# Optimization experiments

Measured on AMD Instinct MI355X. Metric: run time of the kernel, lower is better.

## Reference

```python
import jax, jax.numpy as jnp
import numpy as np

EMB_DIM = 256
Q_DIM = 512
V_DIM = 512

def setup_inputs() -> dict:
    key = jax.random.key(0)
    ks = jax.random.split(key, 7)
    B, S = 8, 2048
    x = jax.random.normal(ks[0], (B, S, EMB_DIM), dtype=jnp.float32)
    s = 1.0 / np.sqrt(EMB_DIM)
    Wq = jax.random.normal(ks[1], (EMB_DIM, Q_DIM), dtype=jnp.float32) * s
    bq = jax.random.normal(ks[2], (Q_DIM,), dtype=jnp.float32) * 0.01
    Wk = jax.random.normal(ks[3], (EMB_DIM, Q_DIM), dtype=jnp.float32) * s
    bk = jax.random.normal(ks[4], (Q_DIM,), dtype=jnp.float32) * 0.01
    Wv = jax.random.normal(ks[5], (EMB_DIM, V_DIM), dtype=jnp.float32) * s
    bv = jax.random.normal(ks[6], (V_DIM,), dtype=jnp.float32) * 0.01
    return {"x": x, "Wq": Wq, "bq": bq, "Wk": Wk, "bk": bk, "Wv": Wv, "bv": bv}

def reference(x, Wq, bq, Wk, bk, Wv, bv):
    # q/k/v projections (torch Linear == x @ W + b with W stored [in, out] here)
    q = jax.nn.sigmoid(jnp.einsum('bse,eq->bsq', x, Wq) + bq)   # [B,S,Q]
    k = jnp.einsum('bse,eq->bsq', x, Wk) + bk                   # [B,S,Q]
    v = jnp.einsum('bse,ev->bsv', x, Wv) + bv                   # [B,S,V]
    scale = 1.0 / jnp.sqrt(jnp.float32(EMB_DIM))
    qk = jnp.einsum('bsq,btq->bst', q, k) * scale               # [B,S,S]
    qk = jax.nn.elu(qk)
    attn = jax.nn.softmax(qk, axis=-1)
    return jnp.einsum('bst,btv->bsv', attn, v)                  # [B,S,V]
```

## Files before the change

### kernel.cpp

```cpp
#include <hip/hip_runtime.h>
#include <hip/hip_bf16.h>
#include <math.h>

typedef unsigned short u16;
using short8 = __attribute__((ext_vector_type(8))) short;
using f32x4  = __attribute__((ext_vector_type(4))) float;

#define BK 32


__device__ __forceinline__ u16 f2bf(float f) {
  union { float f; unsigned u; } v; v.f = f;
  unsigned r = v.u + 0x7FFFu + ((v.u >> 16) & 1u);
  return (u16)(r >> 16);
}

__device__ __forceinline__ float fexp(float x) { return __expf(x); }

__device__ __forceinline__ void gld16(const void* g, void* l) {
  __builtin_amdgcn_global_load_lds(
      (const __attribute__((address_space(1))) void*)g,
      (__attribute__((address_space(3))) void*)l,
      16, 0, 0);
}


__device__ __forceinline__ void gemm_core64(const u16* __restrict__ Ag,
                                            const u16* __restrict__ Bg,
                                            int K, int lda, int ldb,
                                            u16* As, u16* Bs,
                                            f32x4 acc[4][4], int w, int l) {
  const int wm = (w & 1) << 6, wn = (w >> 1) << 6;
  const int ln = l & 15, lq = l >> 4;
  const int sr0 = w * 16 + (l >> 2);
  const int sr1 = 64 + sr0;
  const int skp = (l & 3) * 8;
  const int skg = ((l & 3) ^ ((l >> 3) & 3)) * 8;
  const int kro = (lq ^ ((ln >> 1) & 3)) * 8;

#pragma unroll
  for (int mt = 0; mt < 4; mt++)
#pragma unroll
    for (int nt = 0; nt < 4; nt++) acc[mt][nt] = (f32x4)0.0f;

  for (int k0 = 0; k0 < K; k0 += 64) {
    __syncthreads();
    gld16(Ag + (size_t)sr0 * lda + k0 + skg, As + sr0 * BK + skp);
    gld16(Ag + (size_t)sr1 * lda + k0 + skg, As + sr1 * BK + skp);
    gld16(Ag + (size_t)sr0 * lda + k0 + 32 + skg, As + 4096 + sr0 * BK + skp);
    gld16(Ag + (size_t)sr1 * lda + k0 + 32 + skg, As + 4096 + sr1 * BK + skp);
    gld16(Bg + (size_t)sr0 * ldb + k0 + skg, Bs + sr0 * BK + skp);
    gld16(Bg + (size_t)sr1 * ldb + k0 + skg, Bs + sr1 * BK + skp);
    gld16(Bg + (size_t)sr0 * ldb + k0 + 32 + skg, Bs + 4096 + sr0 * BK + skp);
    gld16(Bg + (size_t)sr1 * ldb + k0 + 32 + skg, Bs + 4096 + sr1 * BK + skp);
    __syncthreads();
#pragma unroll
    for (int h = 0; h < 2; h++) {
      const u16* Ah = As + h * 4096;
      const u16* Bh = Bs + h * 4096;
      short8 af[4], bf[4];
#pragma unroll
      for (int mt = 0; mt < 4; mt++)
        af[mt] = *(const short8*)(Ah + (wm + mt * 16 + ln) * BK + kro);
#pragma unroll
      for (int nt = 0; nt < 4; nt++)
        bf[nt] = *(const short8*)(Bh + (wn + nt * 16 + ln) * BK + kro);
#pragma unroll
      for (int mt = 0; mt < 4; mt++)
#pragma unroll
        for (int nt = 0; nt < 4; nt++)
          acc[mt][nt] = __builtin_amdgcn_mfma_f32_16x16x32_bf16(
              af[mt], bf[nt], acc[mt][nt], 0, 0, 0);
    }
  }
}


__global__ __launch_bounds__(256) void k_conv(
    const float* __restrict__ x, u16* __restrict__ xb,
    const float* __restrict__ Wq, const float* __restrict__ Wk,
    const float* __restrict__ Wv, const float* __restrict__ bq,
    const float* __restrict__ bk, const float* __restrict__ bv,
    u16* __restrict__ Wt, float* __restrict__ bcat,
    float* __restrict__ lsum) {
  const int bid = blockIdx.x;
  if (bid < 4096) {
    int i = bid * 256 + threadIdx.x;
    float4 v = ((const float4*)x)[i];
    ushort4 o;
    o.x = f2bf(v.x); o.y = f2bf(v.y); o.z = f2bf(v.z); o.w = f2bf(v.w);
    ((ushort4*)xb)[i] = o;
  } else if (bid < 5632) {
    int i = (bid - 4096) * 256 + threadIdx.x;
    int nn = i >> 8, e = i & 255;
    int sel = nn >> 9, c = nn & 511;
    const float* W = (sel == 0) ? Wq : (sel == 1) ? Wk : Wv;
    Wt[i] = f2bf(W[e * 512 + c]);
    if (e == 0) {
      const float* bb = (sel == 0) ? bq : (sel == 1) ? bk : bv;
      bcat[nn] = bb[c];
    }
  } else {
    int i = (bid - 5632) * 256 + threadIdx.x;
    lsum[i] = 0.0f;
  }
}


__global__ __launch_bounds__(256) void k_proj(
    const u16* __restrict__ xb, const u16* __restrict__ Wt,
    const float* __restrict__ bcat, u16* __restrict__ qb,
    u16* __restrict__ kb, u16* __restrict__ vtb) {
  __shared__ __align__(16) u16 As8[8 * 4096];
  __shared__ __align__(16) u16 Bs[2 * 4096];
  const int bm = blockIdx.y * 128;
  const int bnq = blockIdx.x;
  const int tid = threadIdx.x, w = tid >> 6, l = tid & 63;
  const int wm = (w & 1) << 6, wn = (w >> 1) << 6;
  const int ln = l & 15, lq = l >> 4;
  const int sr0 = w * 16 + (l >> 2);
  const int sr1 = 64 + sr0;
  const int skp = (l & 3) * 8;
  const int skg = ((l & 3) ^ ((l >> 3) & 3)) * 8;
  const int kro = (lq ^ ((ln >> 1) & 3)) * 8;

#pragma unroll
  for (int kw = 0; kw < 8; kw++) {
    gld16(xb + (size_t)(bm + sr0) * 256 + kw * 32 + skg,
          As8 + kw * 4096 + sr0 * BK + skp);
    gld16(xb + (size_t)(bm + sr1) * 256 + kw * 32 + skg,
          As8 + kw * 4096 + sr1 * BK + skp);
  }

  const int b = bm >> 11, t0 = bm & 2047;
  const int cb = bnq * 128;

  for (int p = 0; p < 3; p++) {
    const u16* Bg = Wt + (size_t)(p * 512 + cb) * 256;
    f32x4 acc[4][4];
#pragma unroll
    for (int mt = 0; mt < 4; mt++)
#pragma unroll
      for (int nt = 0; nt < 4; nt++) acc[mt][nt] = (f32x4)0.0f;

#pragma unroll
    for (int it2 = 0; it2 < 4; it2++) {
      __syncthreads();
      gld16(Bg + (size_t)sr0 * 256 + it2 * 64 + skg, Bs + sr0 * BK + skp);
      gld16(Bg + (size_t)sr1 * 256 + it2 * 64 + skg, Bs + sr1 * BK + skp);
      gld16(Bg + (size_t)sr0 * 256 + it2 * 64 + 32 + skg,
            Bs + 4096 + sr0 * BK + skp);
      gld16(Bg + (size_t)sr1 * 256 + it2 * 64 + 32 + skg,
            Bs + 4096 + sr1 * BK + skp);
      __syncthreads();
#pragma unroll
      for (int h = 0; h < 2; h++) {
        const u16* Aw = As8 + (it2 * 2 + h) * 4096;
        const u16* Bh = Bs + h * 4096;
        short8 af[4], bf[4];
#pragma unroll
        for (int mt = 0; mt < 4; mt++)
          af[mt] = *(const short8*)(Aw + (wm + mt * 16 + ln) * BK + kro);
#pragma unroll
        for (int nt = 0; nt < 4; nt++)
          bf[nt] = *(const short8*)(Bh + (wn + nt * 16 + ln) * BK + kro);
#pragma unroll
        for (int mt = 0; mt < 4; mt++)
#pragma unroll
          for (int nt = 0; nt < 4; nt++)
            acc[mt][nt] = __builtin_amdgcn_mfma_f32_16x16x32_bf16(
                af[mt], bf[nt], acc[mt][nt], 0, 0, 0);
      }
    }

    if (p < 2) {
      u16* dst = p ? kb : qb;
#pragma unroll
      for (int mt = 0; mt < 4; mt++)
#pragma unroll
        for (int r = 0; r < 4; r++) {
          int row = bm + wm + mt * 16 + lq * 4 + r;
          ushort4 o;
#pragma unroll
          for (int nt = 0; nt < 4; nt++) {
            int col = wn + nt * 16 + ln;
            float v = acc[mt][nt][r] + bcat[p * 512 + cb + col];
            float ov = (p == 0) ? __builtin_amdgcn_rcpf(1.0f + fexp(-v)) : v;
            ((u16*)&o)[nt] = f2bf(ov);
          }
          *(ushort4*)&dst[(size_t)row * 512 + cb + wn + ln * 4] = o;
        }
    } else {
      u16* tr = As8;
#pragma unroll
      for (int h = 0; h < 2; h++) {
        __syncthreads();
        if ((w & 1) == h) {
#pragma unroll
          for (int mt = 0; mt < 4; mt++)
#pragma unroll
            for (int nt = 0; nt < 4; nt++) {
              int c = wn + nt * 16 + ln;
              float bias = bcat[1024 + cb + c];
#pragma unroll
              for (int r = 0; r < 4; r++) {
                int lr = mt * 16 + lq * 4 + r;
                tr[c * 68 + lr] = f2bf(acc[mt][nt][r] + bias);
              }
            }
        }
        __syncthreads();
        int c2 = tid >> 1, half = tid & 1;
        size_t dbase = ((size_t)b * 512 + cb + c2) * 2048 + t0 + h * 64 + half * 32;
#pragma unroll
        for (int j = 0; j < 4; j++) {
          ushort4 a0 = *(const ushort4*)&tr[c2 * 68 + half * 32 + j * 8];
          ushort4 a1 = *(const ushort4*)&tr[c2 * 68 + half * 32 + j * 8 + 4];
          *(ushort4*)&vtb[dbase + j * 8] = a0;
          *(ushort4*)&vtb[dbase + j * 8 + 4] = a1;
        }
      }
    }
  }
}


__global__ __launch_bounds__(256, 4) void k_qk(const u16* __restrict__ qb,
                                               const u16* __restrict__ kb,
                                               u16* __restrict__ P,
                                               float* __restrict__ lsum) {
  __shared__ __align__(16) u16 As[2 * 4096];
  __shared__ __align__(16) u16 Bs[2 * 4096];
  const int bid = blockIdx.x;
  const int b = bid & 7, t = bid >> 3;
  const int bm = (t >> 4) * 128, bn = (t & 15) * 128;
  const size_t ob = (size_t)b * 2048 * 512;
  const int tid = threadIdx.x, w = tid >> 6, l = tid & 63;
  f32x4 acc[4][4];
  gemm_core64(qb + ob + (size_t)bm * 512, kb + ob + (size_t)bn * 512,
              512, 512, 512, As, Bs, acc, w, l);

  const int wm = (w & 1) << 6, wn = (w >> 1) << 6;
  const int ln = l & 15, lq = l >> 4;
  const float scale = 0.0625f;
#pragma unroll
  for (int mt = 0; mt < 4; mt++)
#pragma unroll
    for (int r = 0; r < 4; r++) {
      int row = bm + wm + mt * 16 + lq * 4 + r;
      float s = 0.0f;
#pragma unroll
      for (int nt = 0; nt < 4; nt++) {
        int col = bn + wn + nt * 16 + ln;
        float v = acc[mt][nt][r] * scale;
        float e = (v > 0.0f) ? v : (fexp(v) - 1.0f);
        float p = fexp(e);
        P[((size_t)b * 2048 + row) * 2048 + col] = f2bf(p);
        s += p;
      }
#pragma unroll
      for (int o = 1; o < 16; o <<= 1) s += __shfl_xor(s, o);
      if (ln == 0) atomicAdd(&lsum[b * 2048 + row], s);
    }
}


__global__ __launch_bounds__(256, 4) void k_pv(const u16* __restrict__ P,
                                               const u16* __restrict__ vtb,
                                               const float* __restrict__ lsum,
                                               float* __restrict__ out) {
  __shared__ __align__(16) u16 As[2 * 4096];
  __shared__ __align__(16) u16 Bs[2 * 4096];
  const int bid = blockIdx.x;
  const int b = bid & 7, t = bid >> 3;
  const int bm = (t >> 2) * 128, bn = (t & 3) * 128;
  const int tid = threadIdx.x, w = tid >> 6, l = tid & 63;
  f32x4 acc[4][4];
  gemm_core64(P  + (size_t)b * 2048 * 2048 + (size_t)bm * 2048,
              vtb + (size_t)b * 512 * 2048 + (size_t)bn * 2048,
              2048, 2048, 2048, As, Bs, acc, w, l);

  const int wm = (w & 1) << 6, wn = (w >> 1) << 6;
  const int ln = l & 15, lq = l >> 4;
#pragma unroll
  for (int mt = 0; mt < 4; mt++)
#pragma unroll
    for (int r = 0; r < 4; r++) {
      int row = bm + wm + mt * 16 + lq * 4 + r;
      float inv = 1.0f / lsum[b * 2048 + row];
#pragma unroll
      for (int nt = 0; nt < 4; nt++) {
        int col = bn + wn + nt * 16 + ln;
        out[((size_t)b * 2048 + row) * 512 + col] = acc[mt][nt][r] * inv;
      }
    }
}


extern "C" void kernel_launch(void* const* d_in, const int* in_sizes, int n_in,
                              void* d_out, int out_size, void* d_ws, size_t ws_size,
                              hipStream_t stream) {
  const float* x  = (const float*)d_in[0];
  const float* Wq = (const float*)d_in[1];
  const float* bq = (const float*)d_in[2];
  const float* Wk = (const float*)d_in[3];
  const float* bk = (const float*)d_in[4];
  const float* Wv = (const float*)d_in[5];
  const float* bv = (const float*)d_in[6];
  float* out = (float*)d_out;
  char* ws = (char*)d_ws;

  u16*  qb   = (u16*)(ws + 0);
  u16*  kb   = (u16*)(ws + 16777216);
  u16*  vtb  = (u16*)(ws + 33554432);
  float* lsum = (float*)(ws + 50331648);
  u16*  P    = (u16*)(ws + 50397184);
  u16*  xb   = (u16*)(ws + 50397184);
  u16*  Wt   = (u16*)(ws + 58785792);
  float* bcat = (float*)(ws + 59572224);

  k_conv<<<5696, 256, 0, stream>>>(x, xb, Wq, Wk, Wv, bq, bk, bv, Wt, bcat, lsum);
  k_proj<<<dim3(4, 128, 1), 256, 0, stream>>>(xb, Wt, bcat, qb, kb, vtb);
  k_qk<<<2048, 256, 0, stream>>>(qb, kb, P, lsum);
  k_pv<<<512, 256, 0, stream>>>(P, vtb, lsum, out);
}
```

Baseline: 200.5 us.

## Split projection kernel across q/k/v grid dimension using shared gemm core

The projection kernel no longer loops over the three q/k/v weight matrices inside one block with the x tile staged once in a large shared buffer. Each projection now gets its own block through a third grid dimension and calls a shared gemm_core64 routine with a smaller shared footprint. This triples the block count and lowers LDS use per block, which should raise occupancy. The cost is that each x tile is loaded three times instead of once.

```diff
diff --git a/kernel.cpp b/kernel.cpp
--- a/kernel.cpp
+++ b/kernel.cpp
@@ -111,114 +111,64 @@
     const u16* __restrict__ xb, const u16* __restrict__ Wt,
     const float* __restrict__ bcat, u16* __restrict__ qb,
     u16* __restrict__ kb, u16* __restrict__ vtb) {
-  __shared__ __align__(16) u16 As8[8 * 4096];
-  __shared__ __align__(16) u16 Bs[2 * 4096];
+  __shared__ __align__(16) u16 S[16384];
   const int bm = blockIdx.y * 128;
-  const int bnq = blockIdx.x;
+  const int cb = blockIdx.x * 128;
+  const int p  = blockIdx.z;
   const int tid = threadIdx.x, w = tid >> 6, l = tid & 63;
   const int wm = (w & 1) << 6, wn = (w >> 1) << 6;
   const int ln = l & 15, lq = l >> 4;
-  const int sr0 = w * 16 + (l >> 2);
-  const int sr1 = 64 + sr0;
-  const int skp = (l & 3) * 8;
-  const int skg = ((l & 3) ^ ((l >> 3) & 3)) * 8;
-  const int kro = (lq ^ ((ln >> 1) & 3)) * 8;
-
-#pragma unroll
-  for (int kw = 0; kw < 8; kw++) {
-    gld16(xb + (size_t)(bm + sr0) * 256 + kw * 32 + skg,
-          As8 + kw * 4096 + sr0 * BK + skp);
-    gld16(xb + (size_t)(bm + sr1) * 256 + kw * 32 + skg,
-          As8 + kw * 4096 + sr1 * BK + skp);
-  }
-
-  const int b = bm >> 11, t0 = bm & 2047;
-  const int cb = bnq * 128;
-
-  for (int p = 0; p < 3; p++) {
-    const u16* Bg = Wt + (size_t)(p * 512 + cb) * 256;
-    f32x4 acc[4][4];
+
+  f32x4 acc[4][4];
+  gemm_core64(xb + (size_t)bm * 256, Wt + (size_t)(p * 512 + cb) * 256,
+              256, 256, 256, S, S + 8192, acc, w, l);
+
+  if (p < 2) {
+    u16* dst = p ? kb : qb;
 #pragma unroll
     for (int mt = 0; mt < 4; mt++)
 #pragma unroll
-      for (int nt = 0; nt < 4; nt++) acc[mt][nt] = (f32x4)0.0f;
-
-#pragma unroll
-    for (int it2 = 0; it2 < 4; it2++) {
+      for (int r = 0; r < 4; r++) {
+        int row = bm + wm + mt * 16 + lq * 4 + r;
+        ushort4 o;
+#pragma unroll
+        for (int nt = 0; nt < 4; nt++) {
+          int col = wn + nt * 16 + ln;
+          float v = acc[mt][nt][r] + bcat[p * 512 + cb + col];
+          float ov = (p == 0) ? __builtin_amdgcn_rcpf(1.0f + fexp(-v)) : v;
+          ((u16*)&o)[nt] = f2bf(ov);
+        }
+        *(ushort4*)&dst[(size_t)row * 512 + cb + wn + ln * 4] = o;
+      }
+  } else {
+    const int b = bm >> 11, t0 = bm & 2047;
+    u16* tr = S;
+#pragma unroll
+    for (int h = 0; h < 2; h++) {
       __syncthreads();
-      gld16(Bg + (size_t)sr0 * 256 + it2 * 64 + skg, Bs + sr0 * BK + skp);
-      gld16(Bg + (size_t)sr1 * 256 + it2 * 64 + skg, Bs + sr1 * BK + skp);
-      gld16(Bg + (size_t)sr0 * 256 + it2 * 64 + 32 + skg,
-            Bs + 4096 + sr0 * BK + skp);
-      gld16(Bg + (size_t)sr1 * 256 + it2 * 64 + 32 + skg,
-            Bs + 4096 + sr1 * BK + skp);
+      if ((w & 1) == h) {
+#pragma unroll
+        for (int mt = 0; mt < 4; mt++)
+#pragma unroll
+          for (int nt = 0; nt < 4; nt++) {
+            int c = wn + nt * 16 + ln;
+            float bias = bcat[1024 + cb + c];
+#pragma unroll
+            for (int r = 0; r < 4; r++) {
+              int lr = mt * 16 + lq * 4 + r;
+              tr[c * 68 + lr] = f2bf(acc[mt][nt][r] + bias);
+            }
+          }
+      }
       __syncthreads();
-#pragma unroll
-      for (int h = 0; h < 2; h++) {
-        const u16* Aw = As8 + (it2 * 2 + h) * 4096;
-        const u16* Bh = Bs + h * 4096;
-        short8 af[4], bf[4];
-#pragma unroll
-        for (int mt = 0; mt < 4; mt++)
-          af[mt] = *(const short8*)(Aw + (wm + mt * 16 + ln) * BK + kro);
-#pragma unroll
-        for (int nt = 0; nt < 4; nt++)
-          bf[nt] = *(const short8*)(Bh + (wn + nt * 16 + ln) * BK + kro);
-#pragma unroll
-        for (int mt = 0; mt < 4; mt++)
-#pragma unroll
-          for (int nt = 0; nt < 4; nt++)
-            acc[mt][nt] = __builtin_amdgcn_mfma_f32_16x16x32_bf16(
-                af[mt], bf[nt], acc[mt][nt], 0, 0, 0);
-      }
-    }
-
-    if (p < 2) {
-      u16* dst = p ? kb : qb;
-#pragma unroll
-      for (int mt = 0; mt < 4; mt++)
-#pragma unroll
-        for (int r = 0; r < 4; r++) {
-          int row = bm + wm + mt * 16 + lq * 4 + r;
-          ushort4 o;
-#pragma unroll
-          for (int nt = 0; nt < 4; nt++) {
-            int col = wn + nt * 16 + ln;
-            float v = acc[mt][nt][r] + bcat[p * 512 + cb + col];
-            float ov = (p == 0) ? __builtin_amdgcn_rcpf(1.0f + fexp(-v)) : v;
-            ((u16*)&o)[nt] = f2bf(ov);
-          }
-          *(ushort4*)&dst[(size_t)row * 512 + cb + wn + ln * 4] = o;
-        }
-    } else {
-      u16* tr = As8;
-#pragma unroll
-      for (int h = 0; h < 2; h++) {
-        __syncthreads();
-        if ((w & 1) == h) {
-#pragma unroll
-          for (int mt = 0; mt < 4; mt++)
-#pragma unroll
-            for (int nt = 0; nt < 4; nt++) {
-              int c = wn + nt * 16 + ln;
-              float bias = bcat[1024 + cb + c];
-#pragma unroll
-              for (int r = 0; r < 4; r++) {
-                int lr = mt * 16 + lq * 4 + r;
-                tr[c * 68 + lr] = f2bf(acc[mt][nt][r] + bias);
-              }
-            }
-        }
-        __syncthreads();
-        int c2 = tid >> 1, half = tid & 1;
-        size_t dbase = ((size_t)b * 512 + cb + c2) * 2048 + t0 + h * 64 + half * 32;
-#pragma unroll
-        for (int j = 0; j < 4; j++) {
-          ushort4 a0 = *(const ushort4*)&tr[c2 * 68 + half * 32 + j * 8];
-          ushort4 a1 = *(const ushort4*)&tr[c2 * 68 + half * 32 + j * 8 + 4];
-          *(ushort4*)&vtb[dbase + j * 8] = a0;
-          *(ushort4*)&vtb[dbase + j * 8 + 4] = a1;
-        }
+      int c2 = tid >> 1, half = tid & 1;
+      size_t dbase = ((size_t)b * 512 + cb + c2) * 2048 + t0 + h * 64 + half * 32;
+#pragma unroll
+      for (int j = 0; j < 4; j++) {
+        ushort4 a0 = *(const ushort4*)&tr[c2 * 68 + half * 32 + j * 8];
+        ushort4 a1 = *(const ushort4*)&tr[c2 * 68 + half * 32 + j * 8 + 4];
+        *(ushort4*)&vtb[dbase + j * 8] = a0;
+        *(ushort4*)&vtb[dbase + j * 8 + 4] = a1;
       }
     }
   }
@@ -320,7 +270,7 @@
   float* bcat = (float*)(ws + 59572224);
 
   k_conv<<<5696, 256, 0, stream>>>(x, xb, Wq, Wk, Wv, bq, bk, bv, Wt, bcat, lsum);
-  k_proj<<<dim3(4, 128, 1), 256, 0, stream>>>(xb, Wt, bcat, qb, kb, vtb);
+  k_proj<<<dim3(4, 128, 3), 256, 0, stream>>>(xb, Wt, bcat, qb, kb, vtb);
   k_qk<<<2048, 256, 0, stream>>>(qb, kb, P, lsum);
   k_pv<<<512, 256, 0, stream>>>(P, vtb, lsum, out);
 }
```

After: 204.7 us. +2.1%, slower.
